# Performance work log

Hardware: AMD Instinct MI355X
Metric: run time of the kernel (lower is better)

Reference implementation:

```python
import jax, jax.numpy as jnp
import numpy as np
import math

SR = 24000
NH = 100      # num_harmonics
NF = 5        # num_formants
HID = 128
TWO_PI = 2.0 * math.pi


def conv1d(x, w, b, groups=1):
    # x: [B,C,T], w: [O, C//groups, K] (torch OIH layout), 'same' padding
    pad = (w.shape[-1] - 1) // 2
    y = jax.lax.conv_general_dilated(
        x, w, window_strides=(1,), padding=[(pad, pad)],
        dimension_numbers=('NCH', 'OIH', 'NCH'), feature_group_count=groups)
    return y + b[None, :, None]


def lrelu(x):
    return jnp.where(x >= 0, x, 0.1 * x)


def interp_linear(x, L):
    # torch F.interpolate(mode='linear', align_corners=False): x [B,C,T] -> [B,C,L]
    B, C, T = x.shape
    pos = (jnp.arange(L, dtype=x.dtype) + 0.5) * (T / L) - 0.5
    pos = jnp.clip(pos, 0.0, float(T - 1))
    lo = jnp.floor(pos).astype(jnp.int32)
    hi = jnp.minimum(lo + 1, T - 1)
    w = pos - lo.astype(x.dtype)
    return x[:, :, lo] * (1.0 - w) + x[:, :, hi] * w


def setup_inputs():
    key = jax.random.key(0)
    ks = jax.random.split(key, 30)
    ki = iter(range(30))
    def p(shape, s=0.05):
        return s * jax.random.normal(ks[next(ki)], shape, jnp.float32)
    B, T, L = 4, 500, 120000
    inp = {}
    # f0 in [80,120) Hz so actual_harmonics == num_harmonics (static shapes, see notes)
    inp['f0'] = 80.0 + 40.0 * jax.random.uniform(ks[next(ki)], (B, T), jnp.float32)
    inp['condition'] = jax.random.normal(ks[next(ki)], (B, HID, T), jnp.float32)
    # harmonic_amplitude_net params
    inp['ha_w1'] = p((HID, 1, 3));   inp['ha_b1'] = p((HID,))
    inp['ha_w2'] = p((256, HID, 1)); inp['ha_b2'] = p((256,))
    inp['ha_w3'] = p((256, 1, 3));   inp['ha_b3'] = p((256,))
    inp['ha_w4'] = p((256, 256, 1)); inp['ha_b4'] = p((256,))
    inp['ha_w5'] = p((NH, 256, 1));  inp['ha_b5'] = p((NH,))
    # formant predictor params
    inp['fm_w1'] = p((256, HID, 3));    inp['fm_b1'] = p((256,))
    inp['fm_w2'] = p((256, 256, 3));    inp['fm_b2'] = p((256,))
    inp['fm_w3'] = p((2 * NF, 256, 1)); inp['fm_b3'] = p((2 * NF,))
    # voice quality predictor params
    inp['vq_w1'] = p((128, HID, 3)); inp['vq_b1'] = p((128,))
    inp['vq_w2'] = p((64, 128, 3));  inp['vq_b2'] = p((64,))
    inp['vq_w3'] = p((3, 64, 1));    inp['vq_b3'] = p((3,))
    inp['audio_length'] = L
    return inp


def reference(f0, condition,
              ha_w1, ha_b1, ha_w2, ha_b2, ha_w3, ha_b3, ha_w4, ha_b4, ha_w5, ha_b5,
              fm_w1, fm_b1, fm_w2, fm_b2, fm_w3, fm_b3,
              vq_w1, vq_b1, vq_w2, vq_b2, vq_w3, vq_b3,
              audio_length):
    B, T = f0.shape
    L = audio_length
    # ---- harmonic_amplitude_net: (dw3 -> pw1 -> lrelu) x2 -> pw1 -> softplus ----
    a = lrelu(conv1d(conv1d(condition, ha_w1, ha_b1, groups=HID), ha_w2, ha_b2))
    a = lrelu(conv1d(conv1d(a, ha_w3, ha_b3, groups=256), ha_w4, ha_b4))
    harmonic_amplitudes = jax.nn.softplus(conv1d(a, ha_w5, ha_b5))  # [B,NH,T]
    # ---- FormantNetwork ----
    fp = conv1d(lrelu(conv1d(lrelu(conv1d(condition, fm_w1, fm_b1)), fm_w2, fm_b2)), fm_w3, fm_b3)
    ff = 200.0 + 3300.0 * jax.nn.sigmoid(fp[:, :NF])        # [B,NF,T]
    fbw = 50.0 + 150.0 * jax.nn.softplus(fp[:, NF:])        # [B,NF,T]
    hidx = jnp.arange(1, NH + 1, dtype=f0.dtype)
    hfreq = hidx[None, :, None] * f0[:, None, :]            # [B,NH,T]
    num = fbw ** 2                                          # [B,NF,T]
    den = (hfreq[:, None] - ff[:, :, None]) ** 2 + num[:, :, None]  # [B,NF,NH,T]
    res = num[:, :, None] / jnp.maximum(den, 1e-5)
    gain = jnp.prod(0.8 + 0.2 * res, axis=1)                # [B,NH,T]
    shaped = harmonic_amplitudes * gain
    # ---- VoiceQualityNetwork ----
    q = jax.nn.sigmoid(conv1d(lrelu(conv1d(lrelu(conv1d(condition, vq_w1, vq_b1)), vq_w2, vq_b2)), vq_w3, vq_b3))
    q_up = interp_linear(q, L)                              # [B,3,L]
    jitter = q_up[:, 0] * 0.05
    shimmer = q_up[:, 1] * 0.15
    breath = q_up[:, 2] * 0.3
    # ---- phase integration + harmonic bank ----
    f0_up = interp_linear(f0[:, None, :], L)[:, 0]          # [B,L]
    phase = jnp.cumsum(TWO_PI * f0_up / SR, axis=1)
    nk1, nk2, nk3 = jax.random.split(jax.random.key(42), 3)
    jphase = phase + jitter * jax.random.normal(nk1, phase.shape, phase.dtype)
    mask = (hidx[None, :, None] * f0_up[:, None, :] < SR / 2).astype(f0.dtype)  # [B,NH,L]
    amps_up = interp_linear(shaped, L)                      # [B,NH,L]
    sig = jnp.sum(amps_up * jnp.sin(jphase[:, None, :] * hidx[None, :, None]) * mask, axis=1)
    # ---- voice qualities: shimmer envelope + breath noise ----
    shim_env = 1.0 + jax.random.normal(nk2, sig.shape, sig.dtype) * shimmer
    out = sig * shim_env + jax.random.normal(nk3, sig.shape, sig.dtype) * breath
    return out
```

## Files before the change

### kernel.cpp

```cpp
#include <hip/hip_runtime.h>
#include <stdint.h>

#define B_ 4
#define T_ 500
#define L_ 120000
#define NH_ 100
#define N1_ 7500
#define N2_ 469
#define N2P_ 7504
#define N3_ 30
#define N3P_ 480
#define N4_ 2
#define N4P_ 32

#define ACT_NONE 0
#define ACT_LRELU 1
#define ACT_SOFTPLUS 2
#define ACT_SIGMOID 3

__host__ __device__ __forceinline__ uint32_t tf_rotl(uint32_t v, int d) {
  return (v << d) | (v >> (32 - d));
}
__host__ __device__ __forceinline__ void tf_block(uint32_t k0, uint32_t k1,
                                                  uint32_t& x0, uint32_t& x1) {
  uint32_t k2 = k0 ^ k1 ^ 0x1BD11BDAu;
  x0 += k0; x1 += k1;
#define TF_R(d) x0 += x1; x1 = tf_rotl(x1, (d)); x1 ^= x0;
  TF_R(13) TF_R(15) TF_R(26) TF_R(6)   x0 += k1; x1 += k2 + 1u;
  TF_R(17) TF_R(29) TF_R(16) TF_R(24)  x0 += k2; x1 += k0 + 2u;
  TF_R(13) TF_R(15) TF_R(26) TF_R(6)   x0 += k0; x1 += k1 + 3u;
  TF_R(17) TF_R(29) TF_R(16) TF_R(24)  x0 += k1; x1 += k2 + 4u;
  TF_R(13) TF_R(15) TF_R(26) TF_R(6)   x0 += k2; x1 += k0 + 5u;
#undef TF_R
}

__device__ __forceinline__ float erfinv_xla(float x) {
  float w = -log1pf(-(x * x));
  float p;
  if (w < 5.0f) {
    w = w - 2.5f;
    p = 2.81022636e-08f;
    p = fmaf(p, w, 3.43273939e-07f);
    p = fmaf(p, w, -3.5233877e-06f);
    p = fmaf(p, w, -4.39150654e-06f);
    p = fmaf(p, w, 0.00021858087f);
    p = fmaf(p, w, -0.00125372503f);
    p = fmaf(p, w, -0.00417768164f);
    p = fmaf(p, w, 0.246640727f);
    p = fmaf(p, w, 1.50140941f);
  } else {
    w = sqrtf(w) - 3.0f;
    p = -0.000200214257f;
    p = fmaf(p, w, 0.000100950558f);
    p = fmaf(p, w, 0.00134934322f);
    p = fmaf(p, w, -0.00367342844f);
    p = fmaf(p, w, 0.00573950773f);
    p = fmaf(p, w, -0.0076224613f);
    p = fmaf(p, w, 0.00943887047f);
    p = fmaf(p, w, 1.00167406f);
    p = fmaf(p, w, 2.83297682f);
  }
  return p * x;
}

__device__ __forceinline__ float jax_normal(uint32_t k0, uint32_t k1, uint32_t e) {
  uint32_t x0 = 0u, x1 = e;
  tf_block(k0, k1, x0, x1);
  uint32_t bits = x0 ^ x1;
  float u = __uint_as_float((bits >> 9) | 0x3f800000u) - 1.0f;
  float v = __fadd_rn(__fmul_rn(u, 2.0f), -0x1.fffffep-1f);
  v = fmaxf(v, -0x1.fffffep-1f);
  return __fmul_rn((float)1.4142135623730951, erfinv_xla(v));
}

__device__ __forceinline__ float sin_acc(float xf) {
  double x = (double)xf;
  double kd = rint(x * 6.3661977236758138e-01);
  double r = fma(-kd, 1.5707963267948966e+00, x);
  r = fma(-kd, 6.1232339957367660e-17, r);
  float rf = (float)r;
  float y = rf * rf;
  float ps = fmaf(y, 2.7557319e-06f, -1.9841270e-04f);
  ps = fmaf(y, ps, 8.3333335e-03f);
  ps = fmaf(y, ps, -0.16666667f);
  float s = fmaf(rf * y, ps, rf);
  float pc = fmaf(y, -2.7557319e-07f, 2.4801587e-05f);
  pc = fmaf(y, pc, -1.3888889e-03f);
  pc = fmaf(y, pc, 4.1666668e-02f);
  pc = fmaf(y, pc, -0.5f);
  float c = fmaf(y, pc, 1.0f);
  int q = ((int)kd) & 3;
  float rs = (q & 1) ? c : s;
  return (q & 2) ? -rs : rs;
}

__device__ __forceinline__ float apply_act(float v, int act) {
  switch (act) {
    case ACT_LRELU:    return v >= 0.0f ? v : 0.1f * v;
    case ACT_SOFTPLUS: return fmaxf(v, 0.0f) + log1pf(expf(-fabsf(v)));
    case ACT_SIGMOID:  return 1.0f / (1.0f + expf(-v));
  }
  return v;
}


__device__ __forceinline__ void conv3_stream(
    const float* __restrict__ x, const float* __restrict__ w,
    const float* __restrict__ bias, float* __restrict__ y,
    int Cin, int Cout, int o0, int act, int b, int t0, float* smem) {
  for (int idx = threadIdx.x; idx < 16 * Cin * 3; idx += 256) {
    int oo = idx / (Cin * 3), r = idx - oo * (Cin * 3);
    float v = (o0 + oo < Cout) ? w[(size_t)(o0 + oo) * Cin * 3 + r] : 0.0f;
    smem[(r / 3) * 48 + oo * 3 + (r % 3)] = v;
  }
  __syncthreads();
  int lane = threadIdx.x & 63, og = threadIdx.x >> 6;
  int t = t0 + lane;
  int obase = o0 + og * 4;
  float acc[4];
#pragma unroll
  for (int i = 0; i < 4; ++i)
    acc[i] = (obase + i < Cout) ? bias[obase + i] : 0.0f;
  if (t < T_) {
    const bool lo_ok = (t > 0), hi_ok = (t < T_ - 1);
    const float* xr = x + (size_t)b * Cin * T_ + t;
#pragma unroll 2
    for (int cc = 0; cc < Cin; ++cc) {
      const float* xc = xr + (size_t)cc * T_;
      float xm = lo_ok ? xc[-1] : 0.0f;
      float x0 = xc[0];
      float xp = hi_ok ? xc[1] : 0.0f;
      const float4* wq = (const float4*)(smem + cc * 48 + og * 12);
      float4 W0 = wq[0], W1 = wq[1], W2 = wq[2];
      float wl[12] = {W0.x, W0.y, W0.z, W0.w, W1.x, W1.y, W1.z, W1.w,
                      W2.x, W2.y, W2.z, W2.w};
#pragma unroll
      for (int i = 0; i < 4; ++i) {
        acc[i] = fmaf(xm, wl[3 * i + 0], acc[i]);
        acc[i] = fmaf(x0, wl[3 * i + 1], acc[i]);
        acc[i] = fmaf(xp, wl[3 * i + 2], acc[i]);
      }
    }
#pragma unroll
    for (int i = 0; i < 4; ++i) {
      int o = obase + i;
      if (o < Cout) y[((size_t)b * Cout + o) * T_ + t] = apply_act(acc[i], act);
    }
  }
}

__device__ __forceinline__ void dwpw_stream(
    const float* __restrict__ x, const float* __restrict__ wd,
    const float* __restrict__ bd, const float* __restrict__ wp,
    const float* __restrict__ bp, float* __restrict__ y,
    int Cin, int Cout, int o0, int act, int b, int t0, float* smem) {
  float* swd = smem;
  float* swp = smem + Cin * 4;
  for (int idx = threadIdx.x; idx < Cin * 4; idx += 256) {
    int cc = idx >> 2, q = idx & 3;
    swd[idx] = (q < 3) ? wd[(size_t)cc * 3 + q] : bd[cc];
  }
  for (int idx = threadIdx.x; idx < 16 * Cin; idx += 256) {
    int oo = idx / Cin, cc = idx - oo * Cin;
    swp[cc * 16 + oo] = (o0 + oo < Cout) ? wp[(size_t)(o0 + oo) * Cin + cc] : 0.0f;
  }
  __syncthreads();
  int lane = threadIdx.x & 63, og = threadIdx.x >> 6;
  int t = t0 + lane;
  int obase = o0 + og * 4;
  float acc[4];
#pragma unroll
  for (int i = 0; i < 4; ++i)
    acc[i] = (obase + i < Cout) ? bp[obase + i] : 0.0f;
  if (t < T_) {
    const bool lo_ok = (t > 0), hi_ok = (t < T_ - 1);
    const float* xr = x + (size_t)b * Cin * T_ + t;
#pragma unroll 2
    for (int cc = 0; cc < Cin; ++cc) {
      const float* xc = xr + (size_t)cc * T_;
      float xm = lo_ok ? xc[-1] : 0.0f;
      float x0 = xc[0];
      float xp = hi_ok ? xc[1] : 0.0f;
      float4 D = *(const float4*)(swd + cc * 4);
      float d = fmaf(xm, D.x, fmaf(x0, D.y, fmaf(xp, D.z, D.w)));
      float4 Wp = *(const float4*)(swp + cc * 16 + og * 4);
      acc[0] = fmaf(d, Wp.x, acc[0]);
      acc[1] = fmaf(d, Wp.y, acc[1]);
      acc[2] = fmaf(d, Wp.z, acc[2]);
      acc[3] = fmaf(d, Wp.w, acc[3]);
    }
#pragma unroll
    for (int i = 0; i < 4; ++i) {
      int o = obase + i;
      if (o < Cout) y[((size_t)b * Cout + o) * T_ + t] = apply_act(acc[i], act);
    }
  }
}

__device__ __forceinline__ void pw_stream(
    const float* __restrict__ x, const float* __restrict__ w,
    const float* __restrict__ bias, float* __restrict__ y,
    int Cin, int Cout, int o0, int act, int b, int t0, float* smem) {
  for (int idx = threadIdx.x; idx < 16 * Cin; idx += 256) {
    int oo = idx / Cin, cc = idx - oo * Cin;
    smem[cc * 16 + oo] = (o0 + oo < Cout) ? w[(size_t)(o0 + oo) * Cin + cc] : 0.0f;
  }
  __syncthreads();
  int lane = threadIdx.x & 63, og = threadIdx.x >> 6;
  int t = t0 + lane;
  int obase = o0 + og * 4;
  float acc[4];
#pragma unroll
  for (int i = 0; i < 4; ++i)
    acc[i] = (obase + i < Cout) ? bias[obase + i] : 0.0f;
  if (t < T_) {
    const float* xr = x + (size_t)b * Cin * T_ + t;
#pragma unroll 4
    for (int cc = 0; cc < Cin; ++cc) {
      float xv = xr[(size_t)cc * T_];
      float4 Wp = *(const float4*)(smem + cc * 16 + og * 4);
      acc[0] = fmaf(xv, Wp.x, acc[0]);
      acc[1] = fmaf(xv, Wp.y, acc[1]);
      acc[2] = fmaf(xv, Wp.z, acc[2]);
      acc[3] = fmaf(xv, Wp.w, acc[3]);
    }
#pragma unroll
    for (int i = 0; i < 4; ++i) {
      int o = obase + i;
      if (o < Cout) y[((size_t)b * Cout + o) * T_ + t] = apply_act(acc[i], act);
    }
  }
}

__device__ void terms_body(const float* __restrict__ f0, float* __restrict__ A1,
                           int base, int stride) {
  const float RINV = (float)(500.0 / 120000.0);
  for (int gid = base; gid < B_ * N1_; gid += stride) {
    int b = gid / N1_, w = gid - b * N1_;
    const float* f0b = f0 + (size_t)b * T_;
    float* a = A1 + (size_t)b * L_ + (size_t)w * 16;
    float S = 0.0f;
    int lbase = w * 16;
    for (int i = 0; i < 16; ++i) {
      int l = lbase + i;
      float pos = __fsub_rn(__fmul_rn(__fadd_rn((float)l, 0.5f), RINV), 0.5f);
      pos = fminf(fmaxf(pos, 0.0f), 499.0f);
      int lo = (int)floorf(pos);
      int hi = lo + 1; hi = hi < (T_ - 1) ? hi : (T_ - 1);
      float wt = __fsub_rn(pos, (float)lo);
      float omw = __fsub_rn(1.0f, wt);
      float f0up = __fadd_rn(__fmul_rn(f0b[lo], omw), __fmul_rn(f0b[hi], wt));
      float trm = __fdiv_rn(__fmul_rn((float)6.283185307179586, f0up), 24000.0f);
      S = __fadd_rn(S, trm);
      a[i] = S;
    }
  }
}

__device__ void rwr_body(const float* __restrict__ A1, float* __restrict__ A2,
                         float* __restrict__ A3, float* __restrict__ A4,
                         float* __restrict__ E5, float* __restrict__ E3o,
                         float* __restrict__ E2o) {
  int tid = threadIdx.x;
  for (int gid = tid; gid < B_ * N2_; gid += 256) {
    int b = gid / N2_, w = gid - b * N2_;
    float S = 0.0f;
    for (int m = 0; m < 16; ++m) {
      int i = w * 16 + m;
      float v = (i < N1_) ? A1[(size_t)b * L_ + (size_t)i * 16 + 15] : 0.0f;
      S = __fadd_rn(S, v);
      A2[(size_t)b * N2P_ + i] = S;
    }
  }
  __syncthreads();
  for (int gid = tid; gid < B_ * N3_; gid += 256) {
    int b = gid / N3_, w = gid - b * N3_;
    float S = 0.0f;
    for (int m = 0; m < 16; ++m) {
      int i = w * 16 + m;
      float v = (i < N2_) ? A2[(size_t)b * N2P_ + (size_t)i * 16 + 15] : 0.0f;
      S = __fadd_rn(S, v);
      A3[(size_t)b * N3P_ + i] = S;
    }
  }
  __syncthreads();
  for (int gid = tid; gid < B_ * N4_; gid += 256) {
    int b = gid / N4_, w = gid - b * N4_;
    float S = 0.0f;
    for (int m = 0; m < 16; ++m) {
      int i = w * 16 + m;
      float v = (i < N3_) ? A3[(size_t)b * N3P_ + (size_t)i * 16 + 15] : 0.0f;
      S = __fadd_rn(S, v);
      A4[(size_t)b * N4P_ + i] = S;
    }
  }
  __syncthreads();
  if (tid < B_) {
    E5[tid * N4_ + 0] = 0.0f;
    E5[tid * N4_ + 1] = A4[(size_t)tid * N4P_ + 15];
  }
  __syncthreads();
  for (int gid = tid; gid < B_ * N3_; gid += 256) {
    int b = gid / N3_, k = gid - b * N3_;
    float v = 0.0f;
    if (k > 0) {
      int i = k - 1;
      v = __fadd_rn(E5[b * N4_ + (i >> 4)], A4[(size_t)b * N4P_ + i]);
    }
    E3o[b * N3_ + k] = v;
  }
  __syncthreads();
  for (int gid = tid; gid < B_ * N2_; gid += 256) {
    int b = gid / N2_, j = gid - b * N2_;
    float v = 0.0f;
    if (j > 0) {
      int i = j - 1;
      v = __fadd_rn(E3o[b * N3_ + (i >> 4)], A3[(size_t)b * N3P_ + i]);
    }
    E2o[b * N2_ + j] = v;
  }
}

__global__ void __launch_bounds__(256) conv_l1(
    const float* __restrict__ cond, const float* __restrict__ f0,
    const float* __restrict__ fw1, const float* __restrict__ fb1,
    const float* __restrict__ vw1, const float* __restrict__ vb1,
    const float* __restrict__ hw1, const float* __restrict__ hb1,
    const float* __restrict__ hw2, const float* __restrict__ hb2,
    float* __restrict__ fmA, float* __restrict__ vqB, float* __restrict__ haB,
    float* __restrict__ A1) {
  __shared__ __align__(16) float smem[6144];
  int yy = blockIdx.y, b = blockIdx.z, t0 = blockIdx.x * 64;
  if (yy < 16) {
    conv3_stream(cond, fw1, fb1, fmA, 128, 256, yy * 16, ACT_LRELU, b, t0, smem);
  } else if (yy < 24) {
    conv3_stream(cond, vw1, vb1, vqB, 128, 128, (yy - 16) * 16, ACT_LRELU, b, t0, smem);
  } else if (yy < 40) {
    dwpw_stream(cond, hw1, hb1, hw2, hb2, haB, 128, 256, (yy - 24) * 16, ACT_LRELU, b, t0, smem);
  } else {
    int base = (blockIdx.z * 8 + blockIdx.x) * 256 + threadIdx.x;
    terms_body(f0, A1, base, 8192);
  }
}

__global__ void __launch_bounds__(256) conv_l2(
    const float* __restrict__ fmA, const float* __restrict__ vqB,
    const float* __restrict__ haB,
    const float* __restrict__ fw2, const float* __restrict__ fb2,
    const float* __restrict__ vw2, const float* __restrict__ vb2,
    const float* __restrict__ hw3, const float* __restrict__ hb3,
    const float* __restrict__ hw4, const float* __restrict__ hb4,
    float* __restrict__ fmC, float* __restrict__ vqC, float* __restrict__ haC,
    const float* __restrict__ A1, float* __restrict__ A2, float* __restrict__ A3,
    float* __restrict__ A4, float* __restrict__ E5, float* __restrict__ E3o,
    float* __restrict__ E2o) {
  __shared__ __align__(16) float smem[12288];
  int yy = blockIdx.y, b = blockIdx.z, t0 = blockIdx.x * 64;
  if (yy < 16) {
    conv3_stream(fmA, fw2, fb2, fmC, 256, 256, yy * 16, ACT_LRELU, b, t0, smem);
  } else if (yy < 20) {
    conv3_stream(vqB, vw2, vb2, vqC, 128, 64, (yy - 16) * 16, ACT_LRELU, b, t0, smem);
  } else if (yy < 36) {
    dwpw_stream(haB, hw3, hb3, hw4, hb4, haC, 256, 256, (yy - 20) * 16, ACT_LRELU, b, t0, smem);
  } else {
    if (blockIdx.x != 0 || blockIdx.z != 0) return;
    rwr_body(A1, A2, A3, A4, E5, E3o, E2o);
  }
}

__global__ void __launch_bounds__(256) conv_l3(
    const float* __restrict__ haC, const float* __restrict__ fmC,
    const float* __restrict__ vqC,
    const float* __restrict__ hw5, const float* __restrict__ hb5,
    const float* __restrict__ fw3, const float* __restrict__ fb3,
    const float* __restrict__ vw3, const float* __restrict__ vb3,
    float* __restrict__ ha, float* __restrict__ fp, float* __restrict__ qv) {
  __shared__ __align__(16) float smem[4096];
  int yy = blockIdx.y, b = blockIdx.z, t0 = blockIdx.x * 64;
  if (yy < 7) {
    pw_stream(haC, hw5, hb5, ha, 256, 100, yy * 16, ACT_SOFTPLUS, b, t0, smem);
  } else if (yy == 7) {
    pw_stream(fmC, fw3, fb3, fp, 256, 10, 0, ACT_NONE, b, t0, smem);
  } else {
    pw_stream(vqC, vw3, vb3, qv, 64, 3, 0, ACT_SIGMOID, b, t0, smem);
  }
}

__global__ void shaped_kernel(const float* __restrict__ ha, const float* __restrict__ fp,
                              const float* __restrict__ f0, float* __restrict__ out) {
  int t = blockIdx.x, b = blockIdx.y, h = threadIdx.x;
  __shared__ float ff[5], nm[5];
  if (h < 10) {
    float v = fp[((size_t)b * 10 + h) * T_ + t];
    if (h < 5) {
      ff[h] = 200.0f + 3300.0f * (1.0f / (1.0f + expf(-v)));
    } else {
      float bw = 50.0f + 150.0f * (fmaxf(v, 0.0f) + log1pf(expf(-fabsf(v))));
      nm[h - 5] = bw * bw;
    }
  }
  __syncthreads();
  if (h >= NH_) return;
  float hfreq = (float)(h + 1) * f0[(size_t)b * T_ + t];
  float g = 1.0f;
  for (int i = 0; i < 5; ++i) {
    float d = hfreq - ff[i];
    float den = d * d + nm[i];
    float res = nm[i] / fmaxf(den, 1e-5f);
    g = g * (0.8f + 0.2f * res);
  }
  out[((size_t)b * NH_ + h) * T_ + t] = ha[((size_t)b * NH_ + h) * T_ + t] * g;
}

__global__ void __launch_bounds__(256) main_kernel(
    const float* __restrict__ A1, const float* __restrict__ A2,
    const float* __restrict__ E2o,
    const float* __restrict__ shaped, const float* __restrict__ q,
    const float* __restrict__ f0, float* __restrict__ out,
    uint32_t k10, uint32_t k11, uint32_t k20, uint32_t k21, uint32_t k30, uint32_t k31) {
  const float RINV = (float)(500.0 / 120000.0);
  int b = blockIdx.y;
  int l0 = blockIdx.x * 256;
  int l = l0 + threadIdx.x;
  __shared__ float ls[4][NH_];
  float p0 = __fsub_rn(__fmul_rn(__fadd_rn((float)l0, 0.5f), RINV), 0.5f);
  p0 = fminf(fmaxf(p0, 0.0f), 499.0f);
  int lo0 = (int)floorf(p0);
  for (int i = threadIdx.x; i < 4 * NH_; i += 256) {
    int j = i / NH_, h = i - j * NH_;
    int col = lo0 + j; col = col < (T_ - 1) ? col : (T_ - 1);
    ls[j][h] = shaped[((size_t)b * NH_ + h) * T_ + col];
  }
  __syncthreads();
  if (l >= L_) return;

  float pos = __fsub_rn(__fmul_rn(__fadd_rn((float)l, 0.5f), RINV), 0.5f);
  pos = fminf(fmaxf(pos, 0.0f), 499.0f);
  int lo = (int)floorf(pos);
  int hi = lo + 1; hi = hi < (T_ - 1) ? hi : (T_ - 1);
  float w = __fsub_rn(pos, (float)lo);
  float omw = __fsub_rn(1.0f, w);

  const float* f0b = f0 + (size_t)b * T_;
  float f0up = __fadd_rn(__fmul_rn(f0b[lo], omw), __fmul_rn(f0b[hi], w));
  const float* qb = q + (size_t)b * 3 * T_;
  float q0 = __fadd_rn(__fmul_rn(qb[lo], omw), __fmul_rn(qb[hi], w));
  float q1 = __fadd_rn(__fmul_rn(qb[T_ + lo], omw), __fmul_rn(qb[T_ + hi], w));
  float q2 = __fadd_rn(__fmul_rn(qb[2 * T_ + lo], omw), __fmul_rn(qb[2 * T_ + hi], w));
  float jit = __fmul_rn(q0, 0.05f);
  float shm = __fmul_rn(q1, 0.15f);
  float brt = __fmul_rn(q2, 0.3f);

  uint32_t e = (uint32_t)(b * L_ + l);
  float n1 = jax_normal(k10, k11, e);
  float n2 = jax_normal(k20, k21, e);
  float n3 = jax_normal(k30, k31, e);

  float e1v = 0.0f;
  int r = l >> 4;
  if (r > 0) {
    int i = r - 1;
    e1v = __fadd_rn(E2o[b * N2_ + (i >> 4)], A2[(size_t)b * N2P_ + i]);
  }
  float phf = __fadd_rn(e1v, A1[(size_t)b * L_ + l]);
  float jph = __fadd_rn(phf, __fmul_rn(jit, n1));

  int jlo = lo - lo0;
  int jhi = hi - lo0; jhi = jhi < 3 ? jhi : 3;

  float acc = 0.0f;
  for (int h = 1; h <= NH_; ++h) {
    float amp = __fadd_rn(__fmul_rn(ls[jlo][h - 1], omw), __fmul_rn(ls[jhi][h - 1], w));
    float hf = (float)h;
    float arg = __fmul_rn(jph, hf);
    float s = sin_acc(arg);
    float m = (__fmul_rn(hf, f0up) < 12000.0f) ? 1.0f : 0.0f;
    acc = __fadd_rn(acc, __fmul_rn(__fmul_rn(amp, s), m));
  }
  float env = __fadd_rn(1.0f, __fmul_rn(n2, shm));
  out[(size_t)b * L_ + l] = __fadd_rn(__fmul_rn(acc, env), __fmul_rn(n3, brt));
}

extern "C" void kernel_launch(void* const* d_in, const int* in_sizes, int n_in,
                              void* d_out, int out_size, void* d_ws, size_t ws_size,
                              hipStream_t stream) {
  const float* f0    = (const float*)d_in[0];
  const float* cond  = (const float*)d_in[1];
  const float* ha_w1 = (const float*)d_in[2];
  const float* ha_b1 = (const float*)d_in[3];
  const float* ha_w2 = (const float*)d_in[4];
  const float* ha_b2 = (const float*)d_in[5];
  const float* ha_w3 = (const float*)d_in[6];
  const float* ha_b3 = (const float*)d_in[7];
  const float* ha_w4 = (const float*)d_in[8];
  const float* ha_b4 = (const float*)d_in[9];
  const float* ha_w5 = (const float*)d_in[10];
  const float* ha_b5 = (const float*)d_in[11];
  const float* fm_w1 = (const float*)d_in[12];
  const float* fm_b1 = (const float*)d_in[13];
  const float* fm_w2 = (const float*)d_in[14];
  const float* fm_b2 = (const float*)d_in[15];
  const float* fm_w3 = (const float*)d_in[16];
  const float* fm_b3 = (const float*)d_in[17];
  const float* vq_w1 = (const float*)d_in[18];
  const float* vq_b1 = (const float*)d_in[19];
  const float* vq_w2 = (const float*)d_in[20];
  const float* vq_b2 = (const float*)d_in[21];
  const float* vq_w3 = (const float*)d_in[22];
  const float* vq_b3 = (const float*)d_in[23];
  float* out = (float*)d_out;

  uint32_t kw[3][2];
  for (uint32_t j = 0; j < 3; ++j) {
    uint32_t x0 = 0u, x1 = j;
    tf_block(0u, 42u, x0, x1);
    kw[j][0] = x0; kw[j][1] = x1;
  }

  float* ws = (float*)d_ws;
  size_t off = 0;
  auto take = [&](size_t n) { float* p = ws + off; off += (n + 3) & ~(size_t)3; return p; };
  float* fmA = take(512000);
  float* haB = take(512000);
  float* fmC = take(512000);
  float* haC = take(512000);
  float* vqB = take(256000);
  float* vqC = take(128000);
  float* A1  = take((size_t)B_ * L_);
  float* A2  = take((size_t)B_ * N2P_);
  float* A3  = take((size_t)B_ * N3P_);
  float* A4  = take((size_t)B_ * N4P_);
  float* E5  = take((size_t)B_ * N4_);
  float* E3o = take((size_t)B_ * N3_);
  float* E2o = take((size_t)B_ * N2_);
  float* ha = fmA;
  float* fp = vqB;
  float* qv = vqB + 20480;
  float* sh = haB;

  conv_l1<<<dim3(8, 41, B_), 256, 0, stream>>>(
      cond, f0, fm_w1, fm_b1, vq_w1, vq_b1, ha_w1, ha_b1, ha_w2, ha_b2,
      fmA, vqB, haB, A1);
  conv_l2<<<dim3(8, 37, B_), 256, 0, stream>>>(
      fmA, vqB, haB, fm_w2, fm_b2, vq_w2, vq_b2, ha_w3, ha_b3, ha_w4, ha_b4,
      fmC, vqC, haC, A1, A2, A3, A4, E5, E3o, E2o);
  conv_l3<<<dim3(8, 9, B_), 256, 0, stream>>>(
      haC, fmC, vqC, ha_w5, ha_b5, fm_w3, fm_b3, vq_w3, vq_b3, ha, fp, qv);
  shaped_kernel<<<dim3(T_, B_), 128, 0, stream>>>(ha, fp, f0, sh);
  main_kernel<<<dim3((L_ + 255) / 256, B_), 256, 0, stream>>>(
      A1, A2, E2o, sh, qv, f0, out,
      kw[0][0], kw[0][1], kw[1][0], kw[1][1], kw[2][0], kw[2][1]);
  (void)in_sizes; (void)n_in; (void)out_size; (void)ws_size;
}
```

Baseline: 328.7 us.

## Stage conv inputs in shared memory with register-prefetched channel chunks

The k=3 and depthwise-pointwise conv layers now load 32-channel chunks of the input time window into shared memory and double-buffer the next chunk's activations and weights through registers. Each thread computes two adjacent time steps, so the per-block time tile grows from 64 to 128 and the grids for the first two conv kernels are halved. This removes the redundant global loads of the three shifted taps and overlaps loading the next chunk with computing the current one. In exchange there are fewer blocks, more registers per thread, and an extra pair of block syncs per chunk.

```diff
diff --git a/kernel.cpp b/kernel.cpp
--- a/kernel.cpp
+++ b/kernel.cpp
@@ -17,6 +17,9 @@
 #define ACT_LRELU 1
 #define ACT_SOFTPLUS 2
 #define ACT_SIGMOID 3
+
+#define CH3 32
+#define SXW3 132
 
 __host__ __device__ __forceinline__ uint32_t tf_rotl(uint32_t v, int d) {
   return (v << d) | (v >> (32 - d));
@@ -104,95 +107,183 @@
 }
 
 
-__device__ __forceinline__ void conv3_stream(
+__device__ __forceinline__ void conv3_tile(
     const float* __restrict__ x, const float* __restrict__ w,
     const float* __restrict__ bias, float* __restrict__ y,
     int Cin, int Cout, int o0, int act, int b, int t0, float* smem) {
-  for (int idx = threadIdx.x; idx < 16 * Cin * 3; idx += 256) {
-    int oo = idx / (Cin * 3), r = idx - oo * (Cin * 3);
-    float v = (o0 + oo < Cout) ? w[(size_t)(o0 + oo) * Cin * 3 + r] : 0.0f;
-    smem[(r / 3) * 48 + oo * 3 + (r % 3)] = v;
-  }
-  __syncthreads();
-  int lane = threadIdx.x & 63, og = threadIdx.x >> 6;
-  int t = t0 + lane;
+  float* sxf = smem;
+  float* swf = smem + CH3 * SXW3;
+  int tid = threadIdx.x;
+  int lane = tid & 63, og = tid >> 6;
+  int tl = 2 * lane;
+  int t = t0 + tl;
   int obase = o0 + og * 4;
-  float acc[4];
-#pragma unroll
-  for (int i = 0; i < 4; ++i)
-    acc[i] = (obase + i < Cout) ? bias[obase + i] : 0.0f;
-  if (t < T_) {
-    const bool lo_ok = (t > 0), hi_ok = (t < T_ - 1);
-    const float* xr = x + (size_t)b * Cin * T_ + t;
-#pragma unroll 2
-    for (int cc = 0; cc < Cin; ++cc) {
-      const float* xc = xr + (size_t)cc * T_;
-      float xm = lo_ok ? xc[-1] : 0.0f;
-      float x0 = xc[0];
-      float xp = hi_ok ? xc[1] : 0.0f;
-      const float4* wq = (const float4*)(smem + cc * 48 + og * 12);
+  float acc[4][2];
+#pragma unroll
+  for (int i = 0; i < 4; ++i) {
+    float bv = (obase + i < Cout) ? bias[obase + i] : 0.0f;
+    acc[i][0] = bv; acc[i][1] = bv;
+  }
+  float rx[17], rw[6];
+  const int nch = Cin / CH3;
+  auto ld = [&](int c) {
+    int cb = c * CH3;
+#pragma unroll
+    for (int k = 0; k < 17; ++k) {
+      int idx = tid + 256 * k;
+      float v = 0.0f;
+      if (idx < CH3 * 130) {
+        int cc = idx / 130, j = idx - cc * 130;
+        int tt = t0 - 1 + j;
+        if (tt >= 0 && tt < T_) v = x[((size_t)b * Cin + cb + cc) * T_ + tt];
+      }
+      rx[k] = v;
+    }
+#pragma unroll
+    for (int k = 0; k < 6; ++k) {
+      int idx = tid + 256 * k;
+      int oo = idx / 96, r = idx - oo * 96;
+      rw[k] = (o0 + oo < Cout) ? w[((size_t)(o0 + oo) * Cin + cb) * 3 + r] : 0.0f;
+    }
+  };
+  ld(0);
+  for (int c = 0; c < nch; ++c) {
+    __syncthreads();
+#pragma unroll
+    for (int k = 0; k < 17; ++k) {
+      int idx = tid + 256 * k;
+      if (idx < CH3 * 130) {
+        int cc = idx / 130, j = idx - cc * 130;
+        sxf[cc * SXW3 + j] = rx[k];
+      }
+    }
+#pragma unroll
+    for (int k = 0; k < 6; ++k) {
+      int idx = tid + 256 * k;
+      int oo = idx / 96, r = idx - oo * 96;
+      swf[(r / 3) * 52 + oo * 3 + (r % 3)] = rw[k];
+    }
+    __syncthreads();
+    if (c + 1 < nch) ld(c + 1);
+    for (int cc = 0; cc < CH3; ++cc) {
+      const float* row = sxf + cc * SXW3 + tl;
+      float2 xa = *(const float2*)row;
+      float2 xb = *(const float2*)(row + 2);
+      const float4* wq = (const float4*)(swf + cc * 52 + og * 12);
       float4 W0 = wq[0], W1 = wq[1], W2 = wq[2];
       float wl[12] = {W0.x, W0.y, W0.z, W0.w, W1.x, W1.y, W1.z, W1.w,
                       W2.x, W2.y, W2.z, W2.w};
 #pragma unroll
       for (int i = 0; i < 4; ++i) {
-        acc[i] = fmaf(xm, wl[3 * i + 0], acc[i]);
-        acc[i] = fmaf(x0, wl[3 * i + 1], acc[i]);
-        acc[i] = fmaf(xp, wl[3 * i + 2], acc[i]);
+        float w0 = wl[3 * i], w1 = wl[3 * i + 1], w2 = wl[3 * i + 2];
+        acc[i][0] = fmaf(xa.x, w0, acc[i][0]);
+        acc[i][0] = fmaf(xa.y, w1, acc[i][0]);
+        acc[i][0] = fmaf(xb.x, w2, acc[i][0]);
+        acc[i][1] = fmaf(xa.y, w0, acc[i][1]);
+        acc[i][1] = fmaf(xb.x, w1, acc[i][1]);
+        acc[i][1] = fmaf(xb.y, w2, acc[i][1]);
       }
     }
-#pragma unroll
-    for (int i = 0; i < 4; ++i) {
-      int o = obase + i;
-      if (o < Cout) y[((size_t)b * Cout + o) * T_ + t] = apply_act(acc[i], act);
-    }
-  }
-}
-
-__device__ __forceinline__ void dwpw_stream(
+  }
+#pragma unroll
+  for (int i = 0; i < 4; ++i) {
+    int o = obase + i;
+    if (o < Cout) {
+      if (t < T_)     y[((size_t)b * Cout + o) * T_ + t]     = apply_act(acc[i][0], act);
+      if (t + 1 < T_) y[((size_t)b * Cout + o) * T_ + t + 1] = apply_act(acc[i][1], act);
+    }
+  }
+}
+
+__device__ __forceinline__ void dwpw_tile(
     const float* __restrict__ x, const float* __restrict__ wd,
     const float* __restrict__ bd, const float* __restrict__ wp,
     const float* __restrict__ bp, float* __restrict__ y,
     int Cin, int Cout, int o0, int act, int b, int t0, float* smem) {
-  float* swd = smem;
-  float* swp = smem + Cin * 4;
-  for (int idx = threadIdx.x; idx < Cin * 4; idx += 256) {
-    int cc = idx >> 2, q = idx & 3;
-    swd[idx] = (q < 3) ? wd[(size_t)cc * 3 + q] : bd[cc];
-  }
-  for (int idx = threadIdx.x; idx < 16 * Cin; idx += 256) {
-    int oo = idx / Cin, cc = idx - oo * Cin;
-    swp[cc * 16 + oo] = (o0 + oo < Cout) ? wp[(size_t)(o0 + oo) * Cin + cc] : 0.0f;
-  }
-  __syncthreads();
-  int lane = threadIdx.x & 63, og = threadIdx.x >> 6;
-  int t = t0 + lane;
+  float* sxf  = smem;
+  float* swdf = smem + CH3 * SXW3;
+  float* swpf = swdf + CH3 * 4;
+  int tid = threadIdx.x;
+  int lane = tid & 63, og = tid >> 6;
+  int tl = 2 * lane;
+  int t = t0 + tl;
   int obase = o0 + og * 4;
-  float acc[4];
-#pragma unroll
-  for (int i = 0; i < 4; ++i)
-    acc[i] = (obase + i < Cout) ? bp[obase + i] : 0.0f;
-  if (t < T_) {
-    const bool lo_ok = (t > 0), hi_ok = (t < T_ - 1);
-    const float* xr = x + (size_t)b * Cin * T_ + t;
-#pragma unroll 2
-    for (int cc = 0; cc < Cin; ++cc) {
-      const float* xc = xr + (size_t)cc * T_;
-      float xm = lo_ok ? xc[-1] : 0.0f;
-      float x0 = xc[0];
-      float xp = hi_ok ? xc[1] : 0.0f;
-      float4 D = *(const float4*)(swd + cc * 4);
-      float d = fmaf(xm, D.x, fmaf(x0, D.y, fmaf(xp, D.z, D.w)));
-      float4 Wp = *(const float4*)(swp + cc * 16 + og * 4);
-      acc[0] = fmaf(d, Wp.x, acc[0]);
-      acc[1] = fmaf(d, Wp.y, acc[1]);
-      acc[2] = fmaf(d, Wp.z, acc[2]);
-      acc[3] = fmaf(d, Wp.w, acc[3]);
-    }
-#pragma unroll
-    for (int i = 0; i < 4; ++i) {
-      int o = obase + i;
-      if (o < Cout) y[((size_t)b * Cout + o) * T_ + t] = apply_act(acc[i], act);
+  float acc[4][2];
+#pragma unroll
+  for (int i = 0; i < 4; ++i) {
+    float bv = (obase + i < Cout) ? bp[obase + i] : 0.0f;
+    acc[i][0] = bv; acc[i][1] = bv;
+  }
+  float rx[17], rwp[2], rwd1 = 0.0f;
+  const int nch = Cin / CH3;
+  auto ld = [&](int c) {
+    int cb = c * CH3;
+#pragma unroll
+    for (int k = 0; k < 17; ++k) {
+      int idx = tid + 256 * k;
+      float v = 0.0f;
+      if (idx < CH3 * 130) {
+        int cc = idx / 130, j = idx - cc * 130;
+        int tt = t0 - 1 + j;
+        if (tt >= 0 && tt < T_) v = x[((size_t)b * Cin + cb + cc) * T_ + tt];
+      }
+      rx[k] = v;
+    }
+    if (tid < CH3 * 4) {
+      int cc = tid >> 2, q = tid & 3;
+      rwd1 = (q < 3) ? wd[(size_t)(cb + cc) * 3 + q] : bd[cb + cc];
+    }
+#pragma unroll
+    for (int k = 0; k < 2; ++k) {
+      int idx = tid + 256 * k;
+      int oo = idx >> 5, cc = idx & 31;
+      rwp[k] = (o0 + oo < Cout) ? wp[(size_t)(o0 + oo) * Cin + cb + cc] : 0.0f;
+    }
+  };
+  ld(0);
+  for (int c = 0; c < nch; ++c) {
+    __syncthreads();
+#pragma unroll
+    for (int k = 0; k < 17; ++k) {
+      int idx = tid + 256 * k;
+      if (idx < CH3 * 130) {
+        int cc = idx / 130, j = idx - cc * 130;
+        sxf[cc * SXW3 + j] = rx[k];
+      }
+    }
+    if (tid < CH3 * 4) swdf[tid] = rwd1;
+#pragma unroll
+    for (int k = 0; k < 2; ++k) {
+      int idx = tid + 256 * k;
+      int oo = idx >> 5, cc = idx & 31;
+      swpf[cc * 16 + oo] = rwp[k];
+    }
+    __syncthreads();
+    if (c + 1 < nch) ld(c + 1);
+    for (int cc = 0; cc < CH3; ++cc) {
+      const float* row = sxf + cc * SXW3 + tl;
+      float2 xa = *(const float2*)row;
+      float2 xb = *(const float2*)(row + 2);
+      float4 D = *(const float4*)(swdf + cc * 4);
+      float d0 = fmaf(xa.x, D.x, fmaf(xa.y, D.y, fmaf(xb.x, D.z, D.w)));
+      float d1 = fmaf(xa.y, D.x, fmaf(xb.x, D.y, fmaf(xb.y, D.z, D.w)));
+      float4 Wp = *(const float4*)(swpf + cc * 16 + og * 4);
+      acc[0][0] = fmaf(d0, Wp.x, acc[0][0]);
+      acc[1][0] = fmaf(d0, Wp.y, acc[1][0]);
+      acc[2][0] = fmaf(d0, Wp.z, acc[2][0]);
+      acc[3][0] = fmaf(d0, Wp.w, acc[3][0]);
+      acc[0][1] = fmaf(d1, Wp.x, acc[0][1]);
+      acc[1][1] = fmaf(d1, Wp.y, acc[1][1]);
+      acc[2][1] = fmaf(d1, Wp.z, acc[2][1]);
+      acc[3][1] = fmaf(d1, Wp.w, acc[3][1]);
+    }
+  }
+#pragma unroll
+  for (int i = 0; i < 4; ++i) {
+    int o = obase + i;
+    if (o < Cout) {
+      if (t < T_)     y[((size_t)b * Cout + o) * T_ + t]     = apply_act(acc[i][0], act);
+      if (t + 1 < T_) y[((size_t)b * Cout + o) * T_ + t + 1] = apply_act(acc[i][1], act);
     }
   }
 }
@@ -329,17 +420,17 @@
     const float* __restrict__ hw2, const float* __restrict__ hb2,
     float* __restrict__ fmA, float* __restrict__ vqB, float* __restrict__ haB,
     float* __restrict__ A1) {
-  __shared__ __align__(16) float smem[6144];
-  int yy = blockIdx.y, b = blockIdx.z, t0 = blockIdx.x * 64;
+  __shared__ __align__(16) float smem[CH3 * SXW3 + CH3 * 52];
+  int yy = blockIdx.y, b = blockIdx.z, t0 = blockIdx.x * 128;
   if (yy < 16) {
-    conv3_stream(cond, fw1, fb1, fmA, 128, 256, yy * 16, ACT_LRELU, b, t0, smem);
+    conv3_tile(cond, fw1, fb1, fmA, 128, 256, yy * 16, ACT_LRELU, b, t0, smem);
   } else if (yy < 24) {
-    conv3_stream(cond, vw1, vb1, vqB, 128, 128, (yy - 16) * 16, ACT_LRELU, b, t0, smem);
+    conv3_tile(cond, vw1, vb1, vqB, 128, 128, (yy - 16) * 16, ACT_LRELU, b, t0, smem);
   } else if (yy < 40) {
-    dwpw_stream(cond, hw1, hb1, hw2, hb2, haB, 128, 256, (yy - 24) * 16, ACT_LRELU, b, t0, smem);
+    dwpw_tile(cond, hw1, hb1, hw2, hb2, haB, 128, 256, (yy - 24) * 16, ACT_LRELU, b, t0, smem);
   } else {
-    int base = (blockIdx.z * 8 + blockIdx.x) * 256 + threadIdx.x;
-    terms_body(f0, A1, base, 8192);
+    int base = (blockIdx.z * 4 + blockIdx.x) * 256 + threadIdx.x;
+    terms_body(f0, A1, base, 4096);
   }
 }
 
@@ -354,14 +445,14 @@
     const float* __restrict__ A1, float* __restrict__ A2, float* __restrict__ A3,
     float* __restrict__ A4, float* __restrict__ E5, float* __restrict__ E3o,
     float* __restrict__ E2o) {
-  __shared__ __align__(16) float smem[12288];
-  int yy = blockIdx.y, b = blockIdx.z, t0 = blockIdx.x * 64;
+  __shared__ __align__(16) float smem[CH3 * SXW3 + CH3 * 52];
+  int yy = blockIdx.y, b = blockIdx.z, t0 = blockIdx.x * 128;
   if (yy < 16) {
-    conv3_stream(fmA, fw2, fb2, fmC, 256, 256, yy * 16, ACT_LRELU, b, t0, smem);
+    conv3_tile(fmA, fw2, fb2, fmC, 256, 256, yy * 16, ACT_LRELU, b, t0, smem);
   } else if (yy < 20) {
-    conv3_stream(vqB, vw2, vb2, vqC, 128, 64, (yy - 16) * 16, ACT_LRELU, b, t0, smem);
+    conv3_tile(vqB, vw2, vb2, vqC, 128, 64, (yy - 16) * 16, ACT_LRELU, b, t0, smem);
   } else if (yy < 36) {
-    dwpw_stream(haB, hw3, hb3, hw4, hb4, haC, 256, 256, (yy - 20) * 16, ACT_LRELU, b, t0, smem);
+    dwpw_tile(haB, hw3, hb3, hw4, hb4, haC, 256, 256, (yy - 20) * 16, ACT_LRELU, b, t0, smem);
   } else {
     if (blockIdx.x != 0 || blockIdx.z != 0) return;
     rwr_body(A1, A2, A3, A4, E5, E3o, E2o);
@@ -538,10 +629,10 @@
   float* qv = vqB + 20480;
   float* sh = haB;
 
-  conv_l1<<<dim3(8, 41, B_), 256, 0, stream>>>(
+  conv_l1<<<dim3(4, 41, B_), 256, 0, stream>>>(
       cond, f0, fm_w1, fm_b1, vq_w1, vq_b1, ha_w1, ha_b1, ha_w2, ha_b2,
       fmA, vqB, haB, A1);
-  conv_l2<<<dim3(8, 37, B_), 256, 0, stream>>>(
+  conv_l2<<<dim3(4, 37, B_), 256, 0, stream>>>(
       fmA, vqB, haB, fm_w2, fm_b2, vq_w2, vq_b2, ha_w3, ha_b3, ha_w4, ha_b4,
       fmC, vqC, haC, A1, A2, A3, A4, E5, E3o, E2o);
   conv_l3<<<dim3(8, 9, B_), 256, 0, stream>>>(
```

After: 278.1 us. -15.4%, faster.
